# Optimization experiments

Hardware: AMD Instinct MI355X
Metric: run time of the kernel (lower is better)

## Reference

```python
import jax, jax.numpy as jnp
import numpy as np

BETA = 1.0
CODEBOOK_SIZE = 8192
EMBED_DIM = 512


def setup_inputs() -> dict:
    key = jax.random.key(0)
    k1, k2 = jax.random.split(key)
    z = jax.random.normal(k1, (32768, EMBED_DIM), dtype=jnp.float32)
    # Codebook parameter. The original orthogonalizes rows via Gram-Schmidt and
    # scales by 0.1; for the numeric reference a row-normalized random codebook
    # scaled by 0.1 matches the scale/statistics (init detail, not forward math).
    emb = jax.random.normal(k2, (CODEBOOK_SIZE, EMBED_DIM), dtype=jnp.float32)
    emb = 0.1 * emb / jnp.linalg.norm(emb, axis=1, keepdims=True)
    return {"z": z, "emb": emb}


def reference(z, emb):
    # d[n,k] = ||z_n||^2 + ||e_k||^2 - 2 z_n . e_k   (squared distances)
    d = (
        jnp.sum(z * z, axis=1, keepdims=True)
        + jnp.sum(emb * emb, axis=1)
        - 2.0 * jnp.einsum("nd,kd->nk", z, emb)
    )
    idx = jnp.argmin(d, axis=1)              # [N] int
    z_q = jnp.take(emb, idx, axis=0)         # [N, D] gather
    sg = jax.lax.stop_gradient
    loss = jnp.mean((sg(z_q) - z) ** 2) + BETA * jnp.mean((z_q - sg(z)) ** 2)
    z_q_st = z + sg(z_q - z)                 # straight-through estimator
    return (loss, z_q_st, idx)
```

## Files before the change

kernel.cpp:

```cpp
#include <hip/hip_runtime.h>

typedef unsigned short u16;
typedef __attribute__((ext_vector_type(8))) short short8;
typedef __attribute__((ext_vector_type(4))) float f32x4;
typedef __attribute__((ext_vector_type(8))) u16 u16x8;

#define NROWS 32768
#define NCODES 8192
#define DIM 512
#define KT 16

#define BM 256
#define BN 128
#define NSPLIT 8
#define NT (NCODES / NSPLIT / BN)

#define WB_ZH  ((size_t)0)
#define WB_EH  (WB_ZH + (size_t)NROWS * DIM * 2)
#define WB_TE  (WB_EH + (size_t)NCODES * DIM * 2)
#define WB_K4  (WB_TE + (size_t)NCODES * 4)
#define WB_SSQ (WB_K4 + (size_t)NSPLIT * NROWS * 16)
#define WB_NEED (WB_SSQ + (size_t)NROWS * 4 + 64)

__device__ __forceinline__ u16 f2bf(float x) {
  unsigned u = __float_as_uint(x);
  u += 0x7FFFu + ((u >> 16) & 1u);
  return (u16)(u >> 16);
}
__device__ __forceinline__ void gld16(const void* g, void* l) {
  __builtin_amdgcn_global_load_lds(
      (const __attribute__((address_space(1))) void*)g,
      (__attribute__((address_space(3))) void*)l, 16, 0, 0);
}

__global__ void vq_rownorm(const float* __restrict__ x, float* __restrict__ out,
                           int nrows) {
  int gid  = blockIdx.x * blockDim.x + threadIdx.x;
  int w    = gid >> 6;
  int lane = gid & 63;
  if (w >= nrows) return;
  const float4* row = (const float4*)(x + (size_t)w * DIM);
  float4 a = row[lane];
  float4 b = row[lane + 64];
  float s = a.x * a.x + a.y * a.y + a.z * a.z + a.w * a.w
          + b.x * b.x + b.y * b.y + b.z * b.z + b.w * b.w;
#pragma unroll
  for (int off = 32; off > 0; off >>= 1) s += __shfl_down(s, off);
  if (lane == 0) out[w] = s;
}

__global__ void vq_tobf16(const float* __restrict__ x, u16* __restrict__ hi,
                          int nwaves) {
  int W = blockIdx.x * (blockDim.x >> 6) + (threadIdx.x >> 6);
  if (W >= nwaves) return;
  int lane = threadIdx.x & 63;
  int g = W >> 4, kt = W & (KT - 1);
  int row = g * 16 + (lane & 15);
  int k0  = kt * 32 + (lane >> 4) * 8;
  const float* src = x + (size_t)row * DIM + k0;
  f32x4 a = *(const f32x4*)src;
  f32x4 b = *(const f32x4*)(src + 4);
  float v[8] = {a[0], a[1], a[2], a[3], b[0], b[1], b[2], b[3]};
  u16x8 h;
#pragma unroll
  for (int j = 0; j < 8; ++j) h[j] = f2bf(v[j]);
  *(u16x8*)(hi + ((size_t)W * 64 + lane) * 8) = h;
}

__global__ __launch_bounds__(256, 2) void vq_mfma_top4(
    const u16* __restrict__ zh, const u16* __restrict__ eh,
    const float* __restrict__ te, int4* __restrict__ k4) {
  __shared__ __align__(16) u16 lds[12288];
  u16* Ah = lds;
  u16* Bh = lds + 8192;

  const int tid   = threadIdx.x;
  const int w     = tid >> 6;
  const int lane  = tid & 63;
  const int bx    = blockIdx.x;
  const int split = blockIdx.y;
  const int cb    = split * (NT * BN);

  const size_t laneoff = (size_t)lane * 8;
  const u16* pa = zh + ((size_t)(bx * 16 + w * 4) * KT) * 512 + laneoff;

  int k1[16], k2[16];
#pragma unroll
  for (int s = 0; s < 16; ++s) { k1[s] = 0x7fffffff; k2[s] = 0x7fffffff; }

  for (int nt = 0; nt < NT; ++nt) {
    const int col0 = cb + nt * BN;
    const u16* pb = eh + ((size_t)(col0 >> 4) * KT) * 512 + laneoff;

    float tv2[8];
#pragma unroll
    for (int n = 0; n < 8; ++n) tv2[n] = te[col0 + n * 16 + (lane & 15)] * 2048.0f;

    f32x4 acc[4][8];
#pragma unroll
    for (int m = 0; m < 4; ++m)
#pragma unroll
      for (int n = 0; n < 8; ++n) acc[m][n] = (f32x4){0.f, 0.f, 0.f, 0.f};

    for (int kt = 0; kt < KT; ++kt) {
      __syncthreads();
#pragma unroll
      for (int j = 0; j < 4; ++j)
        gld16(pa + ((size_t)(j * KT + kt)) * 512, Ah + (w * 4 + j) * 512);
#pragma unroll
      for (int j = 0; j < 2; ++j)
        gld16(pb + ((size_t)((2 * w + j) * KT + kt)) * 512, Bh + (2 * w + j) * 512);
      __syncthreads();

      short8 a[4];
#pragma unroll
      for (int m = 0; m < 4; ++m)
        a[m] = *(const short8*)(Ah + (w * 4 + m) * 512 + lane * 8);
#pragma unroll
      for (int n = 0; n < 8; ++n) {
        const short8 b = *(const short8*)(Bh + n * 512 + lane * 8);
#pragma unroll
        for (int m = 0; m < 4; ++m)
          acc[m][n] = __builtin_amdgcn_mfma_f32_16x16x32_bf16(a[m], b, acc[m][n], 0, 0, 0);
      }
    }

#pragma unroll
    for (int m = 0; m < 4; ++m)
#pragma unroll
      for (int n = 0; n < 8; ++n) {
        const int col = col0 + n * 16 + (lane & 15);
#pragma unroll
        for (int q = 0; q < 4; ++q) {
          const float kf = fmaf(acc[m][n][q], -4096.0f, tv2[n]);
          const int ki = (int)kf;
          const int key = (int)((unsigned)ki << 13) + col;
          const int s = m * 4 + q;
          const int hi = max(k1[s], key);
          k1[s] = min(k1[s], key);
          k2[s] = min(k2[s], hi);
        }
      }
  }

  int* dump = (int*)lds;
#pragma unroll
  for (int phase = 0; phase < 2; ++phase) {
    __syncthreads();
#pragma unroll
    for (int m2 = 0; m2 < 2; ++m2) {
      const int m = phase * 2 + m2;
#pragma unroll
      for (int q = 0; q < 4; ++q) {
        const int s = m * 4 + q;
        const int r128 = w * 32 + m2 * 16 + (lane >> 4) * 4 + q;
        dump[(r128 * 16 + (lane & 15)) * 2 + 0] = k1[s];
        dump[(r128 * 16 + (lane & 15)) * 2 + 1] = k2[s];
      }
    }
    __syncthreads();
    if (tid < 128) {
      int t0 = 0x7fffffff, t1 = 0x7fffffff, t2 = 0x7fffffff, t3 = 0x7fffffff;
#pragma unroll
      for (int j = 0; j < 32; ++j) {
        int k = dump[tid * 32 + j];
        int x;
        x = min(t0, k); k = max(t0, k); t0 = x;
        x = min(t1, k); k = max(t1, k); t1 = x;
        x = min(t2, k); k = max(t2, k); t2 = x;
        t3 = min(t3, k);
      }
      const int row = bx * BM + (tid >> 5) * 64 + phase * 32 + (tid & 31);
      k4[(size_t)split * NROWS + row] = make_int4(t0, t1, t2, t3);
    }
  }
}

__global__ void vq_rescore8(const float* __restrict__ z, const float* __restrict__ emb,
                            const float* __restrict__ te, const int4* __restrict__ k4,
                            float* __restrict__ out, float* __restrict__ rowssq) {
  const int row  = (blockIdx.x * blockDim.x + threadIdx.x) >> 6;
  const int lane = threadIdx.x & 63;
  if (row >= NROWS) return;

  int t[8];
#pragma unroll
  for (int j = 0; j < 8; ++j) t[j] = 0x7fffffff;
#pragma unroll
  for (int s = 0; s < NSPLIT; ++s) {
    const int4 kk = k4[(size_t)s * NROWS + row];
    int c[4] = {kk.x, kk.y, kk.z, kk.w};
#pragma unroll
    for (int u = 0; u < 4; ++u) {
      int k = c[u];
#pragma unroll
      for (int j = 0; j < 8; ++j) {
        const int lo = min(t[j], k);
        k = max(t[j], k);
        t[j] = lo;
      }
    }
  }

  int idx[8];
#pragma unroll
  for (int c = 0; c < 8; ++c) idx[c] = t[c] & 8191;

  const f32x4* zr = (const f32x4*)(z + (size_t)row * DIM);
  const f32x4 za = zr[lane], zb = zr[lane + 64];

  f32x4 ea[8], eb[8];
#pragma unroll
  for (int c = 0; c < 8; ++c) {
    const f32x4* er = (const f32x4*)(emb + (size_t)idx[c] * DIM);
    ea[c] = er[lane];
    eb[c] = er[lane + 64];
  }

  float sp = za[0] * za[0] + za[1] * za[1] + za[2] * za[2] + za[3] * za[3]
           + zb[0] * zb[0] + zb[1] * zb[1] + zb[2] * zb[2] + zb[3] * zb[3];
  float p[8];
#pragma unroll
  for (int c = 0; c < 8; ++c)
    p[c] = za[0] * ea[c][0] + za[1] * ea[c][1] + za[2] * ea[c][2] + za[3] * ea[c][3]
         + zb[0] * eb[c][0] + zb[1] * eb[c][1] + zb[2] * eb[c][2] + zb[3] * eb[c][3];

#pragma unroll
  for (int off = 32; off > 0; off >>= 1) {
    sp += __shfl_down(sp, off);
#pragma unroll
    for (int c = 0; c < 8; ++c) p[c] += __shfl_down(p[c], off);
  }
  sp = __shfl(sp, 0);
#pragma unroll
  for (int c = 0; c < 8; ++c) p[c] = __shfl(p[c], 0);

  float bd = (sp + te[idx[0]]) - 2.0f * p[0];
  int   bi = idx[0];
  f32x4 ga = ea[0], gb = eb[0];
#pragma unroll
  for (int c = 1; c < 8; ++c) {
    const float d = (sp + te[idx[c]]) - 2.0f * p[c];
    const bool better = (d < bd) || (d == bd && idx[c] < bi);
    if (better) { bd = d; bi = idx[c]; ga = ea[c]; gb = eb[c]; }
  }

  float* orow = out + 1 + (size_t)row * DIM;
  float lsum = 0.f;
#pragma unroll
  for (int j = 0; j < 4; ++j) {
    const float dv = ga[j] - za[j];
    orow[4 * lane + j] = za[j] + dv;
    lsum += dv * dv;
    const float dw = gb[j] - zb[j];
    orow[256 + 4 * lane + j] = zb[j] + dw;
    lsum += dw * dw;
  }
#pragma unroll
  for (int off = 32; off > 0; off >>= 1) lsum += __shfl_down(lsum, off);
  if (lane == 0) {
    rowssq[row] = lsum;
    out[1 + (size_t)NROWS * DIM + row] = (float)bi;
  }
}

__global__ void vq_finalize(const float* __restrict__ rowssq, float* __restrict__ out) {
  __shared__ float red[16];
  float s = 0.f;
  for (int i = threadIdx.x; i < NROWS; i += 1024) s += rowssq[i];
#pragma unroll
  for (int off = 32; off > 0; off >>= 1) s += __shfl_down(s, off);
  if ((threadIdx.x & 63) == 0) red[threadIdx.x >> 6] = s;
  __syncthreads();
  if (threadIdx.x < 64) {
    float v = (threadIdx.x < 16) ? red[threadIdx.x] : 0.f;
#pragma unroll
    for (int off = 32; off > 0; off >>= 1) v += __shfl_down(v, off);
    if (threadIdx.x == 0) {
      const float m = v / 16777216.0f;
      out[0] = m + m;
    }
  }
}

extern "C" void kernel_launch(void* const* d_in, const int* in_sizes, int n_in,
                              void* d_out, int out_size, void* d_ws, size_t ws_size,
                              hipStream_t stream) {
  const float* z   = (const float*)d_in[0];
  const float* emb = (const float*)d_in[1];
  float* out = (float*)d_out;
  char*  ws  = (char*)d_ws;

  u16*   zh  = (u16*)(ws + WB_ZH);
  u16*   eh  = (u16*)(ws + WB_EH);
  float* te  = (float*)(ws + WB_TE);
  int4*  k4  = (int4*)(ws + WB_K4);
  float* ssq = (float*)(ws + WB_SSQ);

  vq_tobf16<<<(NROWS / 16) * KT / 4, 256, 0, stream>>>(z, zh, (NROWS / 16) * KT);
  vq_tobf16<<<(NCODES / 16) * KT / 4, 256, 0, stream>>>(emb, eh, (NCODES / 16) * KT);
  vq_rownorm<<<NCODES / 4, 256, 0, stream>>>(emb, te, NCODES);

  vq_mfma_top4<<<dim3(NROWS / BM, NSPLIT), 256, 0, stream>>>(zh, eh, te, k4);

  vq_rescore8<<<NROWS / 4, 256, 0, stream>>>(z, emb, te, k4, out, ssq);
  vq_finalize<<<1, 1024, 0, stream>>>(ssq, out);
}
```

Baseline: 481.4 us.

## Double-buffer MFMA top-4 kernel with 512-thread 2x4 warp tiling and async LDS prefetch

Rewrites the distance GEMM kernel to use 512 threads with a 4x2 warp grid over a 256x256 tile. Each step now stages two K-slices into a double-buffered 128KB LDS region, and the next slice's global->LDS loads are issued before computing on the current one, using vmcnt waits in place of full syncthreads. It also adds s_setprio around the MFMA bursts and a rotated-index final top-4 merge. The aim is to hide global load latency and cut the barrier count per K step. In exchange it uses far more LDS, which may limit occupancy to one block per CU despite the launch bounds.

```diff
diff --git a/kernel.cpp b/kernel.cpp
--- a/kernel.cpp
+++ b/kernel.cpp
@@ -11,9 +11,10 @@
 #define KT 16
 
 #define BM 256
-#define BN 128
+#define BN 256
 #define NSPLIT 8
 #define NT (NCODES / NSPLIT / BN)
+#define NU (NT * 8)
 
 #define WB_ZH  ((size_t)0)
 #define WB_EH  (WB_ZH + (size_t)NROWS * DIM * 2)
@@ -67,112 +68,140 @@
   *(u16x8*)(hi + ((size_t)W * 64 + lane) * 8) = h;
 }
 
-__global__ __launch_bounds__(256, 2) void vq_mfma_top4(
+__global__ __launch_bounds__(512, 2) void vq_mfma_top4(
     const u16* __restrict__ zh, const u16* __restrict__ eh,
     const float* __restrict__ te, int4* __restrict__ k4) {
-  __shared__ __align__(16) u16 lds[12288];
-  u16* Ah = lds;
-  u16* Bh = lds + 8192;
-
-  const int tid   = threadIdx.x;
-  const int w     = tid >> 6;
-  const int lane  = tid & 63;
-  const int bx    = blockIdx.x;
+  __shared__ __align__(16) u16 lds[65536];
+
+  const int tid  = threadIdx.x;
+  const int w    = tid >> 6;
+  const int lane = tid & 63;
+  const int wr   = w >> 1;
+  const int wc   = w & 1;
+  const int l15  = lane & 15;
+  const int bx   = blockIdx.x;
   const int split = blockIdx.y;
-  const int cb    = split * (NT * BN);
-
-  const size_t laneoff = (size_t)lane * 8;
-  const u16* pa = zh + ((size_t)(bx * 16 + w * 4) * KT) * 512 + laneoff;
-
+  const int cbg  = split * (NT * 16);
+
+  const size_t laneo = (size_t)lane * 8;
+  const u16* Asrc = zh + ((size_t)bx * 16) * (KT * 512);
+  const u16* Bsrc = eh + ((size_t)cbg) * (KT * 512);
+
+  f32x4 acc[4][8];
   int k1[16], k2[16];
 #pragma unroll
   for (int s = 0; s < 16; ++s) { k1[s] = 0x7fffffff; k2[s] = 0x7fffffff; }
 
-  for (int nt = 0; nt < NT; ++nt) {
-    const int col0 = cb + nt * BN;
-    const u16* pb = eh + ((size_t)(col0 >> 4) * KT) * 512 + laneoff;
-
-    float tv2[8];
-#pragma unroll
-    for (int n = 0; n < 8; ++n) tv2[n] = te[col0 + n * 16 + (lane & 15)] * 2048.0f;
-
-    f32x4 acc[4][8];
-#pragma unroll
-    for (int m = 0; m < 4; ++m)
-#pragma unroll
-      for (int n = 0; n < 8; ++n) acc[m][n] = (f32x4){0.f, 0.f, 0.f, 0.f};
-
-    for (int kt = 0; kt < KT; ++kt) {
-      __syncthreads();
-#pragma unroll
-      for (int j = 0; j < 4; ++j)
-        gld16(pa + ((size_t)(j * KT + kt)) * 512, Ah + (w * 4 + j) * 512);
-#pragma unroll
-      for (int j = 0; j < 2; ++j)
-        gld16(pb + ((size_t)((2 * w + j) * KT + kt)) * 512, Bh + (2 * w + j) * 512);
-      __syncthreads();
-
-      short8 a[4];
+  auto stage = [&](int u, int db) {
+    const int nt = u >> 3, uks = u & 7;
+#pragma unroll
+    for (int j = 0; j < 8; ++j) {
+      const int c = w * 8 + j;
+      if (c < 32) {
+        const int g = c >> 1, kto = c & 1;
+        gld16(Asrc + ((size_t)g * KT + uks * 2 + kto) * 512 + laneo,
+              lds + db * 16384 + c * 512);
+      } else {
+        const int cc = c - 32, cg = cc >> 1, kto = cc & 1;
+        gld16(Bsrc + ((size_t)(nt * 16 + cg) * KT + uks * 2 + kto) * 512 + laneo,
+              lds + 32768 + db * 16384 + cc * 512);
+      }
+    }
+  };
+
+  stage(0, 0);
+
+#pragma unroll 2
+  for (int u = 0; u < NU; ++u) {
+    const int db = u & 1;
+    if (u + 1 < NU) {
+      stage(u + 1, db ^ 1);
+      asm volatile("s_waitcnt vmcnt(8)" ::: "memory");
+    } else {
+      asm volatile("s_waitcnt vmcnt(0)" ::: "memory");
+    }
+    __builtin_amdgcn_s_barrier();
+
+    if ((u & 7) == 0) {
 #pragma unroll
       for (int m = 0; m < 4; ++m)
-        a[m] = *(const short8*)(Ah + (w * 4 + m) * 512 + lane * 8);
+#pragma unroll
+        for (int n = 0; n < 8; ++n) acc[m][n] = (f32x4){0.f, 0.f, 0.f, 0.f};
+    }
+
+    const u16* Ab = lds + db * 16384;
+    const u16* Bb = lds + 32768 + db * 16384;
+    short8 a[4], b[4];
+#pragma unroll
+    for (int ph = 0; ph < 4; ++ph) {
+      const int kss = ph >> 1, nh = ph & 1;
+      if (nh == 0) {
+#pragma unroll
+        for (int m = 0; m < 4; ++m)
+          a[m] = *(const short8*)(Ab + ((wr * 4 + m) * 2 + kss) * 512 + lane * 8);
+      }
+#pragma unroll
+      for (int n = 0; n < 4; ++n)
+        b[n] = *(const short8*)(Bb + ((wc * 8 + nh * 4 + n) * 2 + kss) * 512 + lane * 8);
+      __builtin_amdgcn_s_setprio(1);
+#pragma unroll
+      for (int n = 0; n < 4; ++n)
+#pragma unroll
+        for (int m = 0; m < 4; ++m)
+          acc[m][nh * 4 + n] =
+              __builtin_amdgcn_mfma_f32_16x16x32_bf16(a[m], b[n], acc[m][nh * 4 + n], 0, 0, 0);
+      __builtin_amdgcn_s_setprio(0);
+      __builtin_amdgcn_s_barrier();
+    }
+
+    if ((u & 7) == 7) {
+      const int nt = u >> 3;
+      const int colt0 = split * (NT * 256) + nt * 256 + wc * 128 + l15;
 #pragma unroll
       for (int n = 0; n < 8; ++n) {
-        const short8 b = *(const short8*)(Bh + n * 512 + lane * 8);
+        const int col = colt0 + n * 16;
+        const float tv2 = te[col] * 2048.0f;
 #pragma unroll
         for (int m = 0; m < 4; ++m)
-          acc[m][n] = __builtin_amdgcn_mfma_f32_16x16x32_bf16(a[m], b, acc[m][n], 0, 0, 0);
+#pragma unroll
+          for (int q = 0; q < 4; ++q) {
+            const float kf = fmaf(acc[m][n][q], -4096.0f, tv2);
+            const int key = (int)((unsigned)(int)kf << 13) + col;
+            const int s = m * 4 + q;
+            const int hi = max(k1[s], key);
+            k1[s] = min(k1[s], key);
+            k2[s] = min(k2[s], hi);
+          }
       }
     }
-
-#pragma unroll
-    for (int m = 0; m < 4; ++m)
-#pragma unroll
-      for (int n = 0; n < 8; ++n) {
-        const int col = col0 + n * 16 + (lane & 15);
-#pragma unroll
-        for (int q = 0; q < 4; ++q) {
-          const float kf = fmaf(acc[m][n][q], -4096.0f, tv2[n]);
-          const int ki = (int)kf;
-          const int key = (int)((unsigned)ki << 13) + col;
-          const int s = m * 4 + q;
-          const int hi = max(k1[s], key);
-          k1[s] = min(k1[s], key);
-          k2[s] = min(k2[s], hi);
-        }
-      }
-  }
-
-  int* dump = (int*)lds;
-#pragma unroll
-  for (int phase = 0; phase < 2; ++phase) {
-    __syncthreads();
-#pragma unroll
-    for (int m2 = 0; m2 < 2; ++m2) {
-      const int m = phase * 2 + m2;
-#pragma unroll
-      for (int q = 0; q < 4; ++q) {
-        const int s = m * 4 + q;
-        const int r128 = w * 32 + m2 * 16 + (lane >> 4) * 4 + q;
-        dump[(r128 * 16 + (lane & 15)) * 2 + 0] = k1[s];
-        dump[(r128 * 16 + (lane & 15)) * 2 + 1] = k2[s];
-      }
-    }
-    __syncthreads();
-    if (tid < 128) {
-      int t0 = 0x7fffffff, t1 = 0x7fffffff, t2 = 0x7fffffff, t3 = 0x7fffffff;
-#pragma unroll
-      for (int j = 0; j < 32; ++j) {
-        int k = dump[tid * 32 + j];
-        int x;
-        x = min(t0, k); k = max(t0, k); t0 = x;
-        x = min(t1, k); k = max(t1, k); t1 = x;
-        x = min(t2, k); k = max(t2, k); t2 = x;
-        t3 = min(t3, k);
-      }
-      const int row = bx * BM + (tid >> 5) * 64 + phase * 32 + (tid & 31);
-      k4[(size_t)split * NROWS + row] = make_int4(t0, t1, t2, t3);
-    }
+  }
+
+  __builtin_amdgcn_s_barrier();
+  int* di = (int*)lds;
+#pragma unroll
+  for (int m = 0; m < 4; ++m)
+#pragma unroll
+    for (int q = 0; q < 4; ++q) {
+      const int s = m * 4 + q;
+      const int r = wr * 64 + m * 16 + (lane >> 4) * 4 + q;
+      const int base = r * 64 + wc * 32 + l15 * 2;
+      di[base] = k1[s];
+      di[base + 1] = k2[s];
+    }
+  __builtin_amdgcn_s_barrier();
+  if (tid < 256) {
+    int t0 = 0x7fffffff, t1 = 0x7fffffff, t2 = 0x7fffffff, t3 = 0x7fffffff;
+#pragma unroll
+    for (int j = 0; j < 64; ++j) {
+      const int jj = (j + tid) & 63;
+      int k = di[tid * 64 + jj];
+      int x;
+      x = min(t0, k); k = max(t0, k); t0 = x;
+      x = min(t1, k); k = max(t1, k); t1 = x;
+      x = min(t2, k); k = max(t2, k); t2 = x;
+      t3 = min(t3, k);
+    }
+    k4[(size_t)split * NROWS + bx * 256 + tid] = make_int4(t0, t1, t2, t3);
   }
 }
 
@@ -301,7 +330,7 @@
   vq_tobf16<<<(NCODES / 16) * KT / 4, 256, 0, stream>>>(emb, eh, (NCODES / 16) * KT);
   vq_rownorm<<<NCODES / 4, 256, 0, stream>>>(emb, te, NCODES);
 
-  vq_mfma_top4<<<dim3(NROWS / BM, NSPLIT), 256, 0, stream>>>(zh, eh, te, k4);
+  vq_mfma_top4<<<dim3(NROWS / BM, NSPLIT), 512, 0, stream>>>(zh, eh, te, k4);
 
   vq_rescore8<<<NROWS / 4, 256, 0, stream>>>(z, emb, te, k4, out, ssq);
   vq_finalize<<<1, 1024, 0, stream>>>(ssq, out);
```

New measurement: 637.9 us. 1.33x slower.
